# Performance work log

Measured on AMD Instinct MI355X. Metric: run time of the kernel, lower is better.

The kernel has to match this reference:

```python
import jax, jax.numpy as jnp
import numpy as np

D = 64        # input_dim == hidden dims
D2 = 2 * D    # transformer model dim
N = 20000     # num_nodes
R = 24        # num_relation
S = 3         # history snapshots
E = 60000     # edges per snapshot
B = 8         # batch
K = 101       # candidates (1 pos + 100 neg)
HLEN = 50     # history length
NL_GNN = 2
NL_TF = 2
NH = 2        # attention heads
HD = D2 // NH


def setup_inputs() -> dict:
    key = jax.random.key(0)
    ks = list(jax.random.split(key, 40))
    nrm = lambda i, shape: jax.random.normal(ks[i], shape, jnp.float32) * 0.05
    inp = {}
    # embeddings / params
    inp["poi_emb"] = nrm(0, (N, D))
    inp["query_emb"] = nrm(1, (R, D))
    inp["gate_W"] = nrm(2, (D, D)); inp["gate_b"] = jnp.zeros((D,), jnp.float32)
    inp["gnn_rel"] = nrm(3, (NL_GNN, R, D))
    inp["gnn_W"] = nrm(4, (NL_GNN, 2 * D, D)); inp["gnn_b"] = jnp.zeros((NL_GNN, D), jnp.float32)
    inp["g_time_emb"] = nrm(5, (48, D))
    inp["g_lin_W"] = nrm(6, (D, D)); inp["g_lin_b"] = jnp.zeros((D,), jnp.float32)
    inp["tf_Wqkv"] = nrm(7, (NL_TF, D2, 3 * D2))
    inp["tf_Wo"] = nrm(8, (NL_TF, D2, D2))
    ln = jnp.stack([jnp.ones((NL_TF, D2), jnp.float32), jnp.zeros((NL_TF, D2), jnp.float32)], axis=1)
    inp["tf_ln1"] = ln; inp["tf_ln2"] = ln
    inp["tf_W1"] = nrm(9, (NL_TF, D2, 4 * D2)); inp["tf_b1"] = jnp.zeros((NL_TF, 4 * D2), jnp.float32)
    inp["tf_W2"] = nrm(10, (NL_TF, 4 * D2, D2)); inp["tf_b2"] = jnp.zeros((NL_TF, D2), jnp.float32)
    F_DIM = D + D2  # hidden_dims[-1] + 2*input_dim
    inp["mlp_W1"] = nrm(11, (F_DIM, F_DIM)); inp["mlp_b1"] = jnp.zeros((F_DIM,), jnp.float32)
    inp["mlp_W2"] = nrm(12, (F_DIM, 1)); inp["mlp_b2"] = jnp.zeros((1,), jnp.float32)
    inp["history_time_encoding"] = nrm(13, (B, HLEN, D2))
    # graph / index inputs
    inp["edge_src"] = jax.random.randint(ks[14], (S, E), 0, N)
    inp["edge_dst"] = jax.random.randint(ks[15], (S, E), 0, N)
    inp["edge_type"] = jax.random.randint(ks[16], (S, E), 0, R)
    inp["h_index"] = jax.random.randint(ks[17], (B,), 0, N)
    inp["r_index"] = jax.random.randint(ks[18], (B,), 0, R)
    inp["t_index"] = jax.random.randint(ks[19], (B, K), 0, N)
    inp["history_poi"] = jax.random.randint(ks[20], (B, HLEN), 0, N)
    inp["g_time"] = jax.random.randint(ks[21], (S,), 0, 48)
    return inp


def _layer_norm(x, scale, bias):
    m = x.mean(-1, keepdims=True)
    v = ((x - m) ** 2).mean(-1, keepdims=True)
    return (x - m) * jax.lax.rsqrt(v + 1e-5) * scale + bias


def reference(poi_emb, query_emb, gate_W, gate_b, gnn_rel, gnn_W, gnn_b,
              g_time_emb, g_lin_W, g_lin_b,
              tf_Wqkv, tf_Wo, tf_ln1, tf_W1, tf_b1, tf_W2, tf_b2, tf_ln2,
              mlp_W1, mlp_b1, mlp_W2, mlp_b2,
              history_time_encoding,
              edge_src, edge_dst, edge_type, h_index, r_index, t_index,
              history_poi, g_time):
    query = query_emb[r_index]  # [B, D]  (r_index constant across candidates)
    output = jnp.zeros((B, N, D), poi_emb.dtype)
    for s in range(S):  # temporal snapshot loop (memory_update per snapshot)
        src, dst, et = edge_src[s], edge_dst[s], edge_type[s]
        # scatter_add of poi embeddings over both endpoints; identical per batch row
        poi_node = jnp.concatenate([src, dst])  # [2E]
        init_one = jax.ops.segment_sum(poi_emb[poi_node], poi_node, num_segments=N)  # [N, D]
        init = jnp.broadcast_to(init_one[None], (B, N, D))
        if s > 0:
            gate = jax.nn.sigmoid(output @ gate_W + gate_b)  # sigmoid gating vs prior state
            init = init * gate + (1.0 - gate) * output
        x = init
        for l in range(NL_GNN):  # PathAggNet stack: transe message + scatter-sum + linear
            msg = x[:, src] + gnn_rel[l][et][None]  # [B, E, D]
            agg = jnp.zeros((B, N, D), x.dtype).at[:, dst].add(msg)  # [B, N, D]
            x = jax.nn.relu(jnp.concatenate([agg, init], axis=-1) @ gnn_W[l] + gnn_b[l])
        output = x
        query = (query + g_time_emb[g_time[s]][None]) @ g_lin_W + g_lin_b
    feature = output  # [B, N, D]
    r_emb = jnp.broadcast_to(query[:, None], (B, N, D))
    final_feature = jnp.concatenate([feature, r_emb], axis=-1)  # [B, N, 2D]
    # gather history POI features + time encoding -> transformer encoder
    poi_idx = jnp.broadcast_to(history_poi[..., None], (B, HLEN, D2))
    xseq = jnp.take_along_axis(final_feature, poi_idx, axis=1) + history_time_encoding  # [B, HLEN, 2D]
    for l in range(NL_TF):
        qkv = xseq @ tf_Wqkv[l]  # [B, HLEN, 3*D2]
        q, k, v = jnp.split(qkv, 3, axis=-1)
        split_heads = lambda t: t.reshape(B, HLEN, NH, HD).transpose(0, 2, 1, 3)
        q, k, v = split_heads(q), split_heads(k), split_heads(v)
        att = jax.nn.softmax(jnp.einsum('bnqd,bnkd->bnqk', q, k) / jnp.sqrt(jnp.float32(HD)), axis=-1)
        o = jnp.einsum('bnqk,bnkd->bnqd', att, v).transpose(0, 2, 1, 3).reshape(B, HLEN, D2) @ tf_Wo[l]
        xseq = _layer_norm(xseq + o, tf_ln1[l, 0], tf_ln1[l, 1])
        ff = jax.nn.relu(xseq @ tf_W1[l] + tf_b1[l]) @ tf_W2[l] + tf_b2[l]
        xseq = _layer_norm(xseq + ff, tf_ln2[l, 0], tf_ln2[l, 1])
    feature_label = xseq.mean(axis=1, keepdims=True)  # [B, 1, 2D]
    t_idx = jnp.broadcast_to(t_index[..., None], (B, K, D))
    feature_t = jnp.take_along_axis(feature, t_idx, axis=1)  # [B, K, D]
    feature_t = jnp.concatenate([feature_t, jnp.broadcast_to(feature_label, (B, K, D2))], axis=-1)
    hmid = jax.nn.relu(feature_t @ mlp_W1 + mlp_b1)
    score = (hmid @ mlp_W2 + mlp_b2).squeeze(-1)  # [B, K]
    return score
```

## Files before the change

### kernel.cpp

```cpp
#include <hip/hip_runtime.h>
#include <hip/hip_bf16.h>
#include <math.h>

#define DD   64
#define DD2  128
#define NN   20000
#define RR   24
#define SS   3
#define EE   60000
#define BB   8
#define KK   101
#define HLENN 50
#define MROWS 20024

__global__ void hist_kernel(const int* __restrict__ src, const int* __restrict__ dst,
                            int* __restrict__ hist, int* __restrict__ deg) {
    int s = blockIdx.y;
    int e = blockIdx.x * 256 + threadIdx.x;
    if (e < EE) {
        int d0 = dst[s * EE + e], s0 = src[s * EE + e];
        atomicAdd(&hist[s * NN + d0], 1);
        atomicAdd(&deg[s * NN + d0], 1);
        atomicAdd(&deg[s * NN + s0], 1);
    }
}

__global__ void scan_kernel(const int* __restrict__ hist, int* __restrict__ rowptr,
                            int* __restrict__ cursor) {
    int s = blockIdx.x, t = threadIdx.x;
    const int* h = hist + s * NN;
    int* rp = rowptr + s * (NN + 1);
    int* cur = cursor + s * NN;
    __shared__ int sp[1024];
    int base = t * 20, sum = 0;
    for (int i = 0; i < 20; ++i) { int idx = base + i; if (idx < NN) sum += h[idx]; }
    sp[t] = sum;
    __syncthreads();
    for (int off = 1; off < 1024; off <<= 1) {
        int v = (t >= off) ? sp[t - off] : 0;
        __syncthreads();
        sp[t] += v;
        __syncthreads();
    }
    int run = sp[t] - sum;
    for (int i = 0; i < 20; ++i) {
        int idx = base + i;
        if (idx < NN) { rp[idx] = run; cur[idx] = run; run += h[idx]; }
    }
    if (t == 1023) rp[NN] = sp[1023];
}

__global__ void place_kernel(const int* __restrict__ src, const int* __restrict__ dst,
                             const int* __restrict__ et, int* __restrict__ cursor,
                             int* __restrict__ colp) {
    int s = blockIdx.y;
    int e = blockIdx.x * 256 + threadIdx.x;
    if (e < EE) {
        int d0 = dst[s * EE + e];
        int pos = atomicAdd(&cursor[s * NN + d0], 1);
        colp[s * EE + pos] = src[s * EE + e] | (et[s * EE + e] << 16);
    }
}

__global__ void init_kernel(const float* __restrict__ poi, const int* __restrict__ deg,
                            const float* __restrict__ gate_W, const float* __restrict__ gate_b,
                            const float* __restrict__ xprev, float* __restrict__ initb,
                            int use_gate) {
    __shared__ float sW[64][64];
    __shared__ float srow[4][64];
    int li = threadIdx.x >> 6, d = threadIdx.x & 63;
    int node = blockIdx.x * 4 + li;
    if (use_gate) {
        for (int i = threadIdx.x; i < 64 * 64; i += 256) sW[i >> 6][i & 63] = gate_W[i];
    }
    float iv = (float)deg[node] * poi[(size_t)node * 64 + d];
    if (use_gate) {
        float ov = xprev[(size_t)node * 64 + d];
        srow[li][d] = ov;
        __syncthreads();
        float acc = gate_b[d];
        #pragma unroll
        for (int k = 0; k < 64; ++k) acc += srow[li][k] * sW[k][d];
        float g = 1.f / (1.f + expf(-acc));
        iv = iv * g + (1.f - g) * ov;
    }
    initb[(size_t)node * 64 + d] = iv;
}

__global__ void gemm64_kernel(const float* __restrict__ A0a, const float* __restrict__ Ar_a,
                              const float* __restrict__ Ba, float* __restrict__ Ca,
                              const float* __restrict__ A0b, const float* __restrict__ Ar_b,
                              const float* __restrict__ Bb, float* __restrict__ Cb) {
    const float* A0 = blockIdx.y ? A0b : A0a;
    const float* Ar = blockIdx.y ? Ar_b : Ar_a;
    const float* B  = blockIdx.y ? Bb  : Ba;
    float* C        = blockIdx.y ? Cb  : Ca;
    __shared__ float sA[64][68];
    __shared__ float sB[64][68];
    int tid = threadIdx.x;
    int row0 = blockIdx.x * 64;
    for (int i = tid; i < 64 * 16; i += 256) {
        int r = i >> 4, cq = i & 15;
        int row = row0 + r;
        float4 v = make_float4(0.f, 0.f, 0.f, 0.f);
        if (row < NN)         v = *(const float4*)(A0 + (size_t)row * 64 + cq * 4);
        else if (row < MROWS) v = *(const float4*)(Ar + (size_t)(row - NN) * 64 + cq * 4);
        *(float4*)&sA[r][cq * 4] = v;
        float4 w = *(const float4*)(B + (size_t)r * 64 + cq * 4);
        *(float4*)&sB[r][cq * 4] = w;
    }
    __syncthreads();
    int tr = tid >> 4, tc = tid & 15;
    float acc[4][4] = {{0.f}};
    #pragma unroll 16
    for (int k = 0; k < 64; ++k) {
        float4 b4 = *(const float4*)&sB[k][tc * 4];
        float a0 = sA[tr * 4 + 0][k];
        float a1 = sA[tr * 4 + 1][k];
        float a2 = sA[tr * 4 + 2][k];
        float a3 = sA[tr * 4 + 3][k];
        acc[0][0] += a0 * b4.x; acc[0][1] += a0 * b4.y; acc[0][2] += a0 * b4.z; acc[0][3] += a0 * b4.w;
        acc[1][0] += a1 * b4.x; acc[1][1] += a1 * b4.y; acc[1][2] += a1 * b4.z; acc[1][3] += a1 * b4.w;
        acc[2][0] += a2 * b4.x; acc[2][1] += a2 * b4.y; acc[2][2] += a2 * b4.z; acc[2][3] += a2 * b4.w;
        acc[3][0] += a3 * b4.x; acc[3][1] += a3 * b4.y; acc[3][2] += a3 * b4.z; acc[3][3] += a3 * b4.w;
    }
    #pragma unroll
    for (int i = 0; i < 4; ++i) {
        int row = row0 + tr * 4 + i;
        if (row < MROWS) {
            *(float4*)(C + (size_t)row * 64 + tc * 4) = make_float4(acc[i][0], acc[i][1], acc[i][2], acc[i][3]);
        }
    }
}

__global__ void fin_kernel(const float* __restrict__ y, const float* __restrict__ z,
                           const int* __restrict__ rowptr, const int* __restrict__ colp,
                           const float* __restrict__ bias, float* __restrict__ xout) {
    __shared__ float srelW[24][64];
    int tid = threadIdx.x;
    for (int i = tid; i < 24 * 64; i += 256) srelW[i >> 6][i & 63] = y[(size_t)NN * 64 + i];
    int d = tid & 63, w = tid >> 6;
    float bb = bias[d];
    __syncthreads();
    int base = blockIdx.x * 16 + w * 4;
    for (int n = 0; n < 4; ++n) {
        int node = base + n;
        float acc = z[(size_t)node * 64 + d] + bb;
        int e0 = rowptr[node], e1 = rowptr[node + 1];
        for (int e = e0; e < e1; ++e) {
            int pack = colp[e];
            acc += y[(size_t)(pack & 0xFFFF) * 64 + d] + srelW[pack >> 16][d];
        }
        xout[(size_t)node * 64 + d] = fmaxf(acc, 0.f);
    }
}

__global__ void queryxseq_kernel(const float* __restrict__ feature,
                                 const float* __restrict__ query_emb,
                                 const int* __restrict__ r_index,
                                 const float* __restrict__ g_time_emb,
                                 const int* __restrict__ g_time,
                                 const float* __restrict__ g_lin_W,
                                 const float* __restrict__ g_lin_b,
                                 const int* __restrict__ history_poi,
                                 const float* __restrict__ hte,
                                 float* __restrict__ xseq) {
    __shared__ float sW[64][64];
    __shared__ float sq[8][64];
    __shared__ float st[8][64];
    int tid = threadIdx.x;
    int b4 = tid >> 6, d = tid & 63;
    for (int i = tid; i < 64 * 64; i += 256) sW[i >> 6][i & 63] = g_lin_W[i];
    for (int bb = b4; bb < BB; bb += 4) sq[bb][d] = query_emb[r_index[bb] * 64 + d];
    __syncthreads();
    for (int s = 0; s < SS; ++s) {
        for (int bb = b4; bb < BB; bb += 4) st[bb][d] = sq[bb][d] + g_time_emb[g_time[s] * 64 + d];
        __syncthreads();
        for (int bb = b4; bb < BB; bb += 4) {
            float acc = g_lin_b[d];
            #pragma unroll
            for (int k = 0; k < 64; ++k) acc += st[bb][k] * sW[k][d];
            sq[bb][d] = acc;
        }
        __syncthreads();
    }
    int p0 = blockIdx.x * 2048;
    for (int p = p0 + tid; p < p0 + 2048; p += 256) {
        int c = p & 127;
        int bt = p >> 7;
        int b = bt / HLENN, t = bt % HLENN;
        float v = (c < 64) ? feature[(size_t)history_poi[b * HLENN + t] * 64 + c]
                           : sq[b][c - 64];
        xseq[p] = v + hte[p];
    }
}

__global__ void qkv4_kernel(const float* __restrict__ xseq, const float* __restrict__ Wqkv,
                            float* __restrict__ qkvb) {
    __shared__ float sx[4][128];
    int tid = threadIdx.x;
    int row0 = blockIdx.x * 4;
    for (int i = tid; i < 512; i += 384) sx[i >> 7][i & 127] = xseq[row0 * 128 + i];
    __syncthreads();
    float a0 = 0.f, a1 = 0.f, a2 = 0.f, a3 = 0.f;
    #pragma unroll 8
    for (int k = 0; k < 128; ++k) {
        float w = Wqkv[k * 384 + tid];
        a0 += sx[0][k] * w; a1 += sx[1][k] * w; a2 += sx[2][k] * w; a3 += sx[3][k] * w;
    }
    qkvb[(row0 + 0) * 384 + tid] = a0;
    qkvb[(row0 + 1) * 384 + tid] = a1;
    qkvb[(row0 + 2) * 384 + tid] = a2;
    qkvb[(row0 + 3) * 384 + tid] = a3;
}

__global__ void attn_kernel(const float* __restrict__ qkv, float* __restrict__ attnout) {
    int b = blockIdx.x >> 1, h = blockIdx.x & 1;
    __shared__ float sq[HLENN][64], sk[HLENN][64], sv[HLENN][64];
    __shared__ float ss[HLENN][HLENN];
    for (int i = threadIdx.x; i < HLENN * 64; i += 256) {
        int t = i >> 6, d = i & 63;
        const float* base = qkv + (size_t)(b * HLENN + t) * 384 + h * 64 + d;
        sq[t][d] = base[0];
        sk[t][d] = base[128];
        sv[t][d] = base[256];
    }
    __syncthreads();
    for (int p = threadIdx.x; p < HLENN * HLENN; p += 256) {
        int i = p / HLENN, j = p % HLENN;
        float acc = 0.f;
        #pragma unroll 8
        for (int d = 0; d < 64; ++d) acc += sq[i][d] * sk[j][d];
        ss[i][j] = acc * 0.125f;
    }
    __syncthreads();
    if (threadIdx.x < HLENN) {
        int i = threadIdx.x;
        float m = -1e30f;
        for (int j = 0; j < HLENN; ++j) m = fmaxf(m, ss[i][j]);
        float sum = 0.f;
        for (int j = 0; j < HLENN; ++j) { float e = expf(ss[i][j] - m); ss[i][j] = e; sum += e; }
        float inv = 1.f / sum;
        for (int j = 0; j < HLENN; ++j) ss[i][j] *= inv;
    }
    __syncthreads();
    for (int p = threadIdx.x; p < HLENN * 64; p += 256) {
        int i = p >> 6, d = p & 63;
        float acc = 0.f;
        for (int j = 0; j < HLENN; ++j) acc += ss[i][j] * sv[j][d];
        attnout[(size_t)(b * HLENN + i) * 128 + h * 64 + d] = acc;
    }
}

__global__ void addLN4_kernel(const float* __restrict__ aout, const float* __restrict__ Wo,
                              const float* __restrict__ ln, float* __restrict__ xseq) {
    __shared__ float sa[4][128];
    __shared__ float sred[4][128];
    int tid = threadIdx.x;
    int r = tid >> 7, c = tid & 127;
    int row0 = blockIdx.x * 4;
    sa[r][c] = aout[(row0 + r) * 128 + c];
    __syncthreads();
    float acc = xseq[(row0 + r) * 128 + c];
    #pragma unroll 8
    for (int k = 0; k < 128; ++k) acc += sa[r][k] * Wo[k * 128 + c];
    sred[r][c] = acc; __syncthreads();
    for (int off = 64; off > 0; off >>= 1) { if (c < off) sred[r][c] += sred[r][c + off]; __syncthreads(); }
    float mean = sred[r][0] * (1.f / 128.f);
    __syncthreads();
    float dx = acc - mean;
    sred[r][c] = dx * dx; __syncthreads();
    for (int off = 64; off > 0; off >>= 1) { if (c < off) sred[r][c] += sred[r][c + off]; __syncthreads(); }
    float var = sred[r][0] * (1.f / 128.f);
    xseq[(row0 + r) * 128 + c] = dx * rsqrtf(var + 1e-5f) * ln[c] + ln[128 + c];
}

__global__ void ffLN4_kernel(const float* __restrict__ xin, const float* __restrict__ W1,
                             const float* __restrict__ b1, const float* __restrict__ W2,
                             const float* __restrict__ b2, const float* __restrict__ ln,
                             float* __restrict__ xout) {
    __shared__ float sx[4][128];
    __shared__ float sh[4][512];
    __shared__ float spart[4][4][128];
    __shared__ float sred[4][128];
    int tid = threadIdx.x;
    int row0 = blockIdx.x * 4;
    { int r = tid >> 7, c = tid & 127; sx[r][c] = xin[(row0 + r) * 128 + c]; }
    __syncthreads();
    {
        float bb = b1[tid];
        float a0 = bb, a1 = bb, a2 = bb, a3 = bb;
        #pragma unroll 8
        for (int k = 0; k < 128; ++k) {
            float w = W1[k * 512 + tid];
            a0 += sx[0][k] * w; a1 += sx[1][k] * w; a2 += sx[2][k] * w; a3 += sx[3][k] * w;
        }
        sh[0][tid] = fmaxf(a0, 0.f); sh[1][tid] = fmaxf(a1, 0.f);
        sh[2][tid] = fmaxf(a2, 0.f); sh[3][tid] = fmaxf(a3, 0.f);
    }
    __syncthreads();
    int kc = tid >> 7, c = tid & 127;
    float p0 = 0.f, p1 = 0.f, p2 = 0.f, p3 = 0.f;
    #pragma unroll 8
    for (int kk = 0; kk < 128; ++kk) {
        int k = kc * 128 + kk;
        float w = W2[k * 128 + c];
        p0 += sh[0][k] * w; p1 += sh[1][k] * w; p2 += sh[2][k] * w; p3 += sh[3][k] * w;
    }
    spart[kc][0][c] = p0; spart[kc][1][c] = p1; spart[kc][2][c] = p2; spart[kc][3][c] = p3;
    __syncthreads();
    int r = kc;
    float acc = b2[c] + spart[0][r][c] + spart[1][r][c] + spart[2][r][c] + spart[3][r][c] + sx[r][c];
    sred[r][c] = acc; __syncthreads();
    for (int off = 64; off > 0; off >>= 1) { if (c < off) sred[r][c] += sred[r][c + off]; __syncthreads(); }
    float mean = sred[r][0] * (1.f / 128.f);
    __syncthreads();
    float dx = acc - mean;
    sred[r][c] = dx * dx; __syncthreads();
    for (int off = 64; off > 0; off >>= 1) { if (c < off) sred[r][c] += sred[r][c + off]; __syncthreads(); }
    float var = sred[r][0] * (1.f / 128.f);
    xout[(row0 + r) * 128 + c] = dx * rsqrtf(var + 1e-5f) * ln[c] + ln[128 + c];
}

__global__ __launch_bounds__(192) void score_kernel(
        const float* __restrict__ feature, const float* __restrict__ xseq,
        const int* __restrict__ t_index,
        const float* __restrict__ W1, const float* __restrict__ b1,
        const float* __restrict__ W2, const float* __restrict__ b2,
        float* __restrict__ score) {
    int b = blockIdx.x / KK, k = blockIdx.x % KK;
    __shared__ float sf[192];
    __shared__ float sred[192];
    int j = threadIdx.x;
    float v;
    if (j < 64) {
        int t = t_index[b * KK + k];
        v = feature[(size_t)t * 64 + j];
    } else {
        int c = j - 64;
        float s = 0.f;
        #pragma unroll
        for (int t = 0; t < HLENN; ++t) s += xseq[(b * HLENN + t) * 128 + c];
        v = s * (1.f / HLENN);
    }
    sf[j] = v;
    __syncthreads();
    float acc = b1[j];
    #pragma unroll 8
    for (int i = 0; i < 192; ++i) acc += sf[i] * W1[i * 192 + j];
    float h = fmaxf(acc, 0.f);
    sred[j] = h * W2[j];
    __syncthreads();
    if (j < 64) sred[j] += sred[j + 64] + sred[j + 128];
    __syncthreads();
    for (int off = 32; off > 0; off >>= 1) { if (j < off) sred[j] += sred[j + off]; __syncthreads(); }
    if (j == 0) score[b * KK + k] = sred[0] + b2[0];
}

extern "C" void kernel_launch(void* const* d_in, const int* in_sizes, int n_in,
                              void* d_out, int out_size, void* d_ws, size_t ws_size,
                              hipStream_t stream) {
    const float* poi_emb   = (const float*)d_in[0];
    const float* query_emb = (const float*)d_in[1];
    const float* gate_W    = (const float*)d_in[2];
    const float* gate_b    = (const float*)d_in[3];
    const float* gnn_rel   = (const float*)d_in[4];
    const float* gnn_W     = (const float*)d_in[5];
    const float* gnn_b     = (const float*)d_in[6];
    const float* g_time_emb= (const float*)d_in[7];
    const float* g_lin_W   = (const float*)d_in[8];
    const float* g_lin_b   = (const float*)d_in[9];
    const float* tf_Wqkv   = (const float*)d_in[10];
    const float* tf_Wo     = (const float*)d_in[11];
    const float* tf_ln1    = (const float*)d_in[12];
    const float* tf_ln2    = (const float*)d_in[13];
    const float* tf_W1     = (const float*)d_in[14];
    const float* tf_b1     = (const float*)d_in[15];
    const float* tf_W2     = (const float*)d_in[16];
    const float* tf_b2     = (const float*)d_in[17];
    const float* mlp_W1    = (const float*)d_in[18];
    const float* mlp_b1    = (const float*)d_in[19];
    const float* mlp_W2    = (const float*)d_in[20];
    const float* mlp_b2    = (const float*)d_in[21];
    const float* hte       = (const float*)d_in[22];
    const int* edge_src    = (const int*)d_in[23];
    const int* edge_dst    = (const int*)d_in[24];
    const int* edge_type   = (const int*)d_in[25];
    const int* r_index     = (const int*)d_in[27];
    const int* t_index     = (const int*)d_in[28];
    const int* history_poi = (const int*)d_in[29];
    const int* g_time      = (const int*)d_in[30];

    float* ws = (float*)d_ws;
    float* xA    = ws;
    float* xB    = xA + 1280000;
    float* initb = xB + 1280000;
    float* y     = initb + 1280000;
    float* z     = y + 20032 * 64;
    float* xseq  = z + 20032 * 64;
    float* qkvb  = xseq + 51200;
    float* aout  = qkvb + 153600;
    int* hist    = (int*)(aout + 51200);
    int* deg     = hist + 3 * NN;
    int* rowptr  = deg + 3 * NN;
    int* cursor  = rowptr + 3 * (NN + 1);
    int* colp    = cursor + 3 * NN;

    hipMemsetAsync(hist, 0, 2 * 3 * NN * sizeof(int), stream);
    {
        dim3 g((EE + 255) / 256, 3);
        hist_kernel<<<g, 256, 0, stream>>>(edge_src, edge_dst, hist, deg);
        scan_kernel<<<3, 1024, 0, stream>>>(hist, rowptr, cursor);
        place_kernel<<<g, 256, 0, stream>>>(edge_src, edge_dst, edge_type, cursor, colp);
    }

    for (int s = 0; s < SS; ++s) {
        const int* rp = rowptr + s * (NN + 1);
        const int* cp = colp + s * EE;
        init_kernel<<<NN / 4, 256, 0, stream>>>(poi_emb, deg + s * NN, gate_W, gate_b,
                                                xA, initb, s > 0 ? 1 : 0);
        const float* Wt0 = gnn_W;
        const float* Wb0 = gnn_W + 64 * 64;
        const float* Wt1 = gnn_W + 128 * 64;
        const float* Wb1 = gnn_W + 128 * 64 + 64 * 64;
        const float* rel0 = gnn_rel;
        const float* rel1 = gnn_rel + 24 * 64;
        dim3 gg(313, 2);
        gemm64_kernel<<<gg, 256, 0, stream>>>(initb, rel0, Wt0, y,
                                              initb, rel0, Wb0, z);
        fin_kernel<<<NN / 16, 256, 0, stream>>>(y, z, rp, cp, gnn_b, xB);
        gemm64_kernel<<<gg, 256, 0, stream>>>(xB, rel1, Wt1, y,
                                              initb, rel1, Wb1, z);
        fin_kernel<<<NN / 16, 256, 0, stream>>>(y, z, rp, cp, gnn_b + 64, xA);
    }

    queryxseq_kernel<<<25, 256, 0, stream>>>(xA, query_emb, r_index, g_time_emb,
                                             g_time, g_lin_W, g_lin_b,
                                             history_poi, hte, xseq);

    for (int l = 0; l < 2; ++l) {
        qkv4_kernel<<<BB * HLENN / 4, 384, 0, stream>>>(xseq, tf_Wqkv + l * 128 * 384, qkvb);
        attn_kernel<<<BB * 2, 256, 0, stream>>>(qkvb, aout);
        addLN4_kernel<<<BB * HLENN / 4, 512, 0, stream>>>(aout, tf_Wo + l * 128 * 128,
                                                          tf_ln1 + l * 256, xseq);
        ffLN4_kernel<<<BB * HLENN / 4, 512, 0, stream>>>(xseq, tf_W1 + l * 128 * 512,
                                                         tf_b1 + l * 512, tf_W2 + l * 512 * 128,
                                                         tf_b2 + l * 128, tf_ln2 + l * 256, xseq);
    }

    score_kernel<<<BB * KK, 192, 0, stream>>>(xA, xseq, t_index,
                                              mlp_W1, mlp_b1, mlp_W2, mlp_b2, (float*)d_out);
}
```

Before: 533.5 us.

## Fuse gate into GNN finalize, batch GEMMs, and fuse transformer output stages

The gated init for the next snapshot moves into a new finGate kernel that runs right after the last GNN layer, so the separate init_kernel with gating goes away. The z GEMMs for both layers are batched into one three-output launch, since both use initb, and this needs an extra z2 buffer. In the transformer, addLN and feed-forward LN are fused into one tfout kernel, and the next layer's QKV projection is folded into its tail. Together these cut the launch count and the global round-trips, at the cost of more shared memory per block.

```diff
diff --git a/kernel.cpp b/kernel.cpp
--- a/kernel.cpp
+++ b/kernel.cpp
@@ -63,38 +63,19 @@
 }
 
 __global__ void init_kernel(const float* __restrict__ poi, const int* __restrict__ deg,
-                            const float* __restrict__ gate_W, const float* __restrict__ gate_b,
-                            const float* __restrict__ xprev, float* __restrict__ initb,
-                            int use_gate) {
-    __shared__ float sW[64][64];
-    __shared__ float srow[4][64];
+                            float* __restrict__ initb) {
     int li = threadIdx.x >> 6, d = threadIdx.x & 63;
     int node = blockIdx.x * 4 + li;
-    if (use_gate) {
-        for (int i = threadIdx.x; i < 64 * 64; i += 256) sW[i >> 6][i & 63] = gate_W[i];
-    }
-    float iv = (float)deg[node] * poi[(size_t)node * 64 + d];
-    if (use_gate) {
-        float ov = xprev[(size_t)node * 64 + d];
-        srow[li][d] = ov;
-        __syncthreads();
-        float acc = gate_b[d];
-        #pragma unroll
-        for (int k = 0; k < 64; ++k) acc += srow[li][k] * sW[k][d];
-        float g = 1.f / (1.f + expf(-acc));
-        iv = iv * g + (1.f - g) * ov;
-    }
-    initb[(size_t)node * 64 + d] = iv;
-}
-
-__global__ void gemm64_kernel(const float* __restrict__ A0a, const float* __restrict__ Ar_a,
-                              const float* __restrict__ Ba, float* __restrict__ Ca,
-                              const float* __restrict__ A0b, const float* __restrict__ Ar_b,
-                              const float* __restrict__ Bb, float* __restrict__ Cb) {
-    const float* A0 = blockIdx.y ? A0b : A0a;
-    const float* Ar = blockIdx.y ? Ar_b : Ar_a;
-    const float* B  = blockIdx.y ? Bb  : Ba;
-    float* C        = blockIdx.y ? Cb  : Ca;
+    initb[(size_t)node * 64 + d] = (float)deg[node] * poi[(size_t)node * 64 + d];
+}
+
+__global__ void gemm64_kernel(const float* __restrict__ A0, const float* __restrict__ Ar,
+                              const float* __restrict__ B0, const float* __restrict__ B1,
+                              const float* __restrict__ B2,
+                              float* __restrict__ C0, float* __restrict__ C1,
+                              float* __restrict__ C2) {
+    const float* B = blockIdx.y == 0 ? B0 : (blockIdx.y == 1 ? B1 : B2);
+    float* C       = blockIdx.y == 0 ? C0 : (blockIdx.y == 1 ? C1 : C2);
     __shared__ float sA[64][68];
     __shared__ float sB[64][68];
     int tid = threadIdx.x;
@@ -155,6 +136,53 @@
     }
 }
 
+__global__ void finGate_kernel(const float* __restrict__ y, const float* __restrict__ z,
+                               const int* __restrict__ rowptr, const int* __restrict__ colp,
+                               const float* __restrict__ bias,
+                               const float* __restrict__ gate_W, const float* __restrict__ gate_b,
+                               const int* __restrict__ deg_next, const float* __restrict__ poi,
+                               float* __restrict__ xout, float* __restrict__ init_next,
+                               int do_gate) {
+    __shared__ float srelW[24][64];
+    __shared__ float sX[16][64];
+    __shared__ float sGW[64][64];
+    int tid = threadIdx.x;
+    for (int i = tid; i < 24 * 64; i += 256) srelW[i >> 6][i & 63] = y[(size_t)NN * 64 + i];
+    if (do_gate) {
+        for (int i = tid; i < 64 * 64; i += 256) sGW[i >> 6][i & 63] = gate_W[i];
+    }
+    int d = tid & 63, w = tid >> 6;
+    float bb = bias[d];
+    __syncthreads();
+    int base = blockIdx.x * 16 + w * 4;
+    for (int n = 0; n < 4; ++n) {
+        int node = base + n;
+        float acc = z[(size_t)node * 64 + d] + bb;
+        int e0 = rowptr[node], e1 = rowptr[node + 1];
+        for (int e = e0; e < e1; ++e) {
+            int pack = colp[e];
+            acc += y[(size_t)(pack & 0xFFFF) * 64 + d] + srelW[pack >> 16][d];
+        }
+        float v = fmaxf(acc, 0.f);
+        xout[(size_t)node * 64 + d] = v;
+        sX[w * 4 + n][d] = v;
+    }
+    if (do_gate) {
+        __syncthreads();
+        float gb = gate_b[d];
+        for (int n = 0; n < 4; ++n) {
+            int ln = w * 4 + n;
+            int node = base + n;
+            float acc = gb;
+            #pragma unroll
+            for (int k = 0; k < 64; ++k) acc += sX[ln][k] * sGW[k][d];
+            float g = 1.f / (1.f + expf(-acc));
+            float iv = (float)deg_next[node] * poi[(size_t)node * 64 + d];
+            init_next[(size_t)node * 64 + d] = iv * g + (1.f - g) * sX[ln][d];
+        }
+    }
+}
+
 __global__ void queryxseq_kernel(const float* __restrict__ feature,
                                  const float* __restrict__ query_emb,
                                  const int* __restrict__ r_index,
@@ -252,13 +280,24 @@
     }
 }
 
-__global__ void addLN4_kernel(const float* __restrict__ aout, const float* __restrict__ Wo,
-                              const float* __restrict__ ln, float* __restrict__ xseq) {
+template<int DO_QKV>
+__global__ __launch_bounds__(512) void tfout_kernel(
+        const float* __restrict__ aout, const float* __restrict__ Wo,
+        const float* __restrict__ ln1,
+        const float* __restrict__ W1, const float* __restrict__ b1,
+        const float* __restrict__ W2, const float* __restrict__ b2,
+        const float* __restrict__ ln2,
+        float* __restrict__ xseq,
+        const float* __restrict__ Wqkv_next, float* __restrict__ qkvb) {
     __shared__ float sa[4][128];
+    __shared__ float sx[4][128];
+    __shared__ float sh[4][512];
+    __shared__ float spart[4][4][128];
     __shared__ float sred[4][128];
-    int tid = threadIdx.x;
+    __shared__ float sfin[4][128];
+    int tid = threadIdx.x;
+    int row0 = blockIdx.x * 4;
     int r = tid >> 7, c = tid & 127;
-    int row0 = blockIdx.x * 4;
     sa[r][c] = aout[(row0 + r) * 128 + c];
     __syncthreads();
     float acc = xseq[(row0 + r) * 128 + c];
@@ -272,20 +311,7 @@
     sred[r][c] = dx * dx; __syncthreads();
     for (int off = 64; off > 0; off >>= 1) { if (c < off) sred[r][c] += sred[r][c + off]; __syncthreads(); }
     float var = sred[r][0] * (1.f / 128.f);
-    xseq[(row0 + r) * 128 + c] = dx * rsqrtf(var + 1e-5f) * ln[c] + ln[128 + c];
-}
-
-__global__ void ffLN4_kernel(const float* __restrict__ xin, const float* __restrict__ W1,
-                             const float* __restrict__ b1, const float* __restrict__ W2,
-                             const float* __restrict__ b2, const float* __restrict__ ln,
-                             float* __restrict__ xout) {
-    __shared__ float sx[4][128];
-    __shared__ float sh[4][512];
-    __shared__ float spart[4][4][128];
-    __shared__ float sred[4][128];
-    int tid = threadIdx.x;
-    int row0 = blockIdx.x * 4;
-    { int r = tid >> 7, c = tid & 127; sx[r][c] = xin[(row0 + r) * 128 + c]; }
+    sx[r][c] = dx * rsqrtf(var + 1e-5f) * ln1[c] + ln1[128 + c];
     __syncthreads();
     {
         float bb = b1[tid];
@@ -299,7 +325,7 @@
         sh[2][tid] = fmaxf(a2, 0.f); sh[3][tid] = fmaxf(a3, 0.f);
     }
     __syncthreads();
-    int kc = tid >> 7, c = tid & 127;
+    int kc = tid >> 7;
     float p0 = 0.f, p1 = 0.f, p2 = 0.f, p3 = 0.f;
     #pragma unroll 8
     for (int kk = 0; kk < 128; ++kk) {
@@ -309,17 +335,33 @@
     }
     spart[kc][0][c] = p0; spart[kc][1][c] = p1; spart[kc][2][c] = p2; spart[kc][3][c] = p3;
     __syncthreads();
-    int r = kc;
-    float acc = b2[c] + spart[0][r][c] + spart[1][r][c] + spart[2][r][c] + spart[3][r][c] + sx[r][c];
-    sred[r][c] = acc; __syncthreads();
+    float acc2 = b2[c] + spart[0][r][c] + spart[1][r][c] + spart[2][r][c] + spart[3][r][c] + sx[r][c];
+    sred[r][c] = acc2; __syncthreads();
     for (int off = 64; off > 0; off >>= 1) { if (c < off) sred[r][c] += sred[r][c + off]; __syncthreads(); }
-    float mean = sred[r][0] * (1.f / 128.f);
-    __syncthreads();
-    float dx = acc - mean;
-    sred[r][c] = dx * dx; __syncthreads();
+    float mean2 = sred[r][0] * (1.f / 128.f);
+    __syncthreads();
+    float dx2 = acc2 - mean2;
+    sred[r][c] = dx2 * dx2; __syncthreads();
     for (int off = 64; off > 0; off >>= 1) { if (c < off) sred[r][c] += sred[r][c + off]; __syncthreads(); }
-    float var = sred[r][0] * (1.f / 128.f);
-    xout[(row0 + r) * 128 + c] = dx * rsqrtf(var + 1e-5f) * ln[c] + ln[128 + c];
+    float var2 = sred[r][0] * (1.f / 128.f);
+    float out = dx2 * rsqrtf(var2 + 1e-5f) * ln2[c] + ln2[128 + c];
+    xseq[(row0 + r) * 128 + c] = out;
+    if (DO_QKV) {
+        sfin[r][c] = out;
+        __syncthreads();
+        if (tid < 384) {
+            float a0 = 0.f, a1 = 0.f, a2 = 0.f, a3 = 0.f;
+            #pragma unroll 8
+            for (int k = 0; k < 128; ++k) {
+                float w = Wqkv_next[k * 384 + tid];
+                a0 += sfin[0][k] * w; a1 += sfin[1][k] * w; a2 += sfin[2][k] * w; a3 += sfin[3][k] * w;
+            }
+            qkvb[(row0 + 0) * 384 + tid] = a0;
+            qkvb[(row0 + 1) * 384 + tid] = a1;
+            qkvb[(row0 + 2) * 384 + tid] = a2;
+            qkvb[(row0 + 3) * 384 + tid] = a3;
+        }
+    }
 }
 
 __global__ __launch_bounds__(192) void score_kernel(
@@ -397,7 +439,8 @@
     float* initb = xB + 1280000;
     float* y     = initb + 1280000;
     float* z     = y + 20032 * 64;
-    float* xseq  = z + 20032 * 64;
+    float* z2    = z + 20032 * 64;
+    float* xseq  = z2 + 20032 * 64;
     float* qkvb  = xseq + 51200;
     float* aout  = qkvb + 153600;
     int* hist    = (int*)(aout + 51200);
@@ -406,6 +449,13 @@
     int* cursor  = rowptr + 3 * (NN + 1);
     int* colp    = cursor + 3 * NN;
 
+    const float* Wt0  = gnn_W;
+    const float* Wb0  = gnn_W + 64 * 64;
+    const float* Wt1  = gnn_W + 128 * 64;
+    const float* Wb1  = gnn_W + 128 * 64 + 64 * 64;
+    const float* rel0 = gnn_rel;
+    const float* rel1 = gnn_rel + 24 * 64;
+
     hipMemsetAsync(hist, 0, 2 * 3 * NN * sizeof(int), stream);
     {
         dim3 g((EE + 255) / 256, 3);
@@ -414,39 +464,35 @@
         place_kernel<<<g, 256, 0, stream>>>(edge_src, edge_dst, edge_type, cursor, colp);
     }
 
+    init_kernel<<<NN / 4, 256, 0, stream>>>(poi_emb, deg, initb);
     for (int s = 0; s < SS; ++s) {
         const int* rp = rowptr + s * (NN + 1);
         const int* cp = colp + s * EE;
-        init_kernel<<<NN / 4, 256, 0, stream>>>(poi_emb, deg + s * NN, gate_W, gate_b,
-                                                xA, initb, s > 0 ? 1 : 0);
-        const float* Wt0 = gnn_W;
-        const float* Wb0 = gnn_W + 64 * 64;
-        const float* Wt1 = gnn_W + 128 * 64;
-        const float* Wb1 = gnn_W + 128 * 64 + 64 * 64;
-        const float* rel0 = gnn_rel;
-        const float* rel1 = gnn_rel + 24 * 64;
-        dim3 gg(313, 2);
-        gemm64_kernel<<<gg, 256, 0, stream>>>(initb, rel0, Wt0, y,
-                                              initb, rel0, Wb0, z);
+        gemm64_kernel<<<dim3(313, 3), 256, 0, stream>>>(initb, rel0,
+                                                        Wt0, Wb0, Wb1, y, z, z2);
         fin_kernel<<<NN / 16, 256, 0, stream>>>(y, z, rp, cp, gnn_b, xB);
-        gemm64_kernel<<<gg, 256, 0, stream>>>(xB, rel1, Wt1, y,
-                                              initb, rel1, Wb1, z);
-        fin_kernel<<<NN / 16, 256, 0, stream>>>(y, z, rp, cp, gnn_b + 64, xA);
+        gemm64_kernel<<<dim3(313, 1), 256, 0, stream>>>(xB, rel1,
+                                                        Wt1, Wt1, Wt1, y, y, y);
+        finGate_kernel<<<NN / 16, 256, 0, stream>>>(
+            y, z2, rp, cp, gnn_b + 64, gate_W, gate_b,
+            deg + (s + 1 < SS ? (s + 1) * NN : 0), poi_emb,
+            xA, initb, s + 1 < SS ? 1 : 0);
     }
 
     queryxseq_kernel<<<25, 256, 0, stream>>>(xA, query_emb, r_index, g_time_emb,
                                              g_time, g_lin_W, g_lin_b,
                                              history_poi, hte, xseq);
 
-    for (int l = 0; l < 2; ++l) {
-        qkv4_kernel<<<BB * HLENN / 4, 384, 0, stream>>>(xseq, tf_Wqkv + l * 128 * 384, qkvb);
-        attn_kernel<<<BB * 2, 256, 0, stream>>>(qkvb, aout);
-        addLN4_kernel<<<BB * HLENN / 4, 512, 0, stream>>>(aout, tf_Wo + l * 128 * 128,
-                                                          tf_ln1 + l * 256, xseq);
-        ffLN4_kernel<<<BB * HLENN / 4, 512, 0, stream>>>(xseq, tf_W1 + l * 128 * 512,
-                                                         tf_b1 + l * 512, tf_W2 + l * 512 * 128,
-                                                         tf_b2 + l * 128, tf_ln2 + l * 256, xseq);
-    }
+    qkv4_kernel<<<BB * HLENN / 4, 384, 0, stream>>>(xseq, tf_Wqkv, qkvb);
+    attn_kernel<<<BB * 2, 256, 0, stream>>>(qkvb, aout);
+    tfout_kernel<1><<<BB * HLENN / 4, 512, 0, stream>>>(
+        aout, tf_Wo, tf_ln1, tf_W1, tf_b1, tf_W2, tf_b2, tf_ln2,
+        xseq, tf_Wqkv + 128 * 384, qkvb);
+    attn_kernel<<<BB * 2, 256, 0, stream>>>(qkvb, aout);
+    tfout_kernel<0><<<BB * HLENN / 4, 512, 0, stream>>>(
+        aout, tf_Wo + 128 * 128, tf_ln1 + 256, tf_W1 + 128 * 512, tf_b1 + 512,
+        tf_W2 + 512 * 128, tf_b2 + 128, tf_ln2 + 256,
+        xseq, nullptr, nullptr);
 
     score_kernel<<<BB * KK, 192, 0, stream>>>(xA, xseq, t_index,
                                               mlp_W1, mlp_b1, mlp_W2, mlp_b2, (float*)d_out);
```

Result: no change. 530.7 us (-0.5%).
